# Kernel optimization log

Hardware: AMD Instinct MI355X
Metric: run time of the kernel (lower is better)

## Reference

```python
import jax, jax.numpy as jnp
import numpy as np

N, IN, WS, OUT, H = 50000, 256, 128, 32, 4
E, M, K = 800000, 2, 10
D = OUT * H  # 128
NEG_SLOPE = 0.2


def _decay(n, alpha=1.5):
    k = np.arange(1, n + 1)
    x = 1.0 / np.power(k, alpha)
    return (x / x.sum()).astype(np.float32)


def setup_inputs() -> dict:
    key = jax.random.key(0)
    ks = jax.random.split(key, 16)
    h = jax.random.normal(ks[0], (N, IN), dtype=jnp.float32)
    src0 = jax.random.randint(ks[1], (E,), 0, N, dtype=jnp.int32)
    dst0 = jax.random.randint(ks[2], (E,), 0, N, dtype=jnp.int32)
    src1 = jax.random.randint(ks[3], (E,), 0, N, dtype=jnp.int32)
    dst1 = jax.random.randint(ks[4], (E,), 0, N, dtype=jnp.int32)
    s = 0.05
    Wh = jax.random.normal(ks[5], (WS, IN), dtype=jnp.float32) * s
    # layer 0 (per metapath): fc (H*F, WS), attn_l/attn_r (H, F)
    fc0 = jax.random.normal(ks[6], (M, H * OUT, WS), dtype=jnp.float32) * s
    al0 = jax.random.normal(ks[7], (M, H, OUT), dtype=jnp.float32) * s
    ar0 = jax.random.normal(ks[8], (M, H, OUT), dtype=jnp.float32) * s
    # layer 1 (per metapath): fc (H*F, H*F)
    fc1 = jax.random.normal(ks[9], (M, H * OUT, H * OUT), dtype=jnp.float32) * s
    al1 = jax.random.normal(ks[10], (M, H, OUT), dtype=jnp.float32) * s
    ar1 = jax.random.normal(ks[11], (M, H, OUT), dtype=jnp.float32) * s
    Wp1 = jax.random.normal(ks[12], (128, D), dtype=jnp.float32) * s
    bp1 = jnp.zeros((128,), dtype=jnp.float32)
    Wp2 = jax.random.normal(ks[13], (1, 128), dtype=jnp.float32) * s
    return dict(h=h, src0=src0, dst0=dst0, src1=src1, dst1=dst1, Wh=Wh,
                fc0=fc0, al0=al0, ar0=ar0, fc1=fc1, al1=al1, ar1=ar1,
                Wp1=Wp1, bp1=bp1, Wp2=Wp2)


def gat_layer(x, src, dst, fcW, attn_l, attn_r):
    # x: (N, Din); fcW: (H*F, Din)
    ft = (x @ fcW.T).reshape(N, H, OUT)            # (N, H, F)
    el = jnp.sum(ft * attn_l, axis=-1)             # (N, H)
    er = jnp.sum(ft * attn_r, axis=-1)             # (N, H)
    e = jax.nn.leaky_relu(el[src] + er[dst], NEG_SLOPE)  # (E, H)
    # edge softmax over incoming edges of each destination node
    mx = jax.ops.segment_max(e, dst, num_segments=N)     # (N, H)
    ee = jnp.exp(e - mx[dst])
    sm = jax.ops.segment_sum(ee, dst, num_segments=N)    # (N, H)
    a = ee / sm[dst]                                     # (E, H)
    # global top-k over the edge dimension (th.topk dim=0), per head
    scores, idx = jax.lax.top_k(a.T, K)                  # (H, K)
    scores = jax.nn.softmax(scores, axis=-1)             # softmax over k
    a_new = jnp.zeros_like(a).at[idx, jnp.arange(H)[:, None]].set(scores)
    msg = ft[src] * a_new[:, :, None]                    # (E, H, F)
    out = jax.ops.segment_sum(msg, dst, num_segments=N)  # (N, H, F)
    return jax.nn.elu(out).reshape(N, H * OUT)


def reference(h, src0, dst0, src1, dst1, Wh, fc0, al0, ar0, fc1, al1, ar1, Wp1, bp1, Wp2):
    c = _decay(2, 1.5)
    wh = h @ Wh.T  # (N, WS)
    srcs = (src0, src1)
    dsts = (dst0, dst1)
    embs = []
    for i in range(M):
        a = gat_layer(wh, srcs[i], dsts[i], fc0[i], al0[i], ar0[i])  # (N, D)
        b = gat_layer(a, srcs[i], dsts[i], fc1[i], al1[i], ar1[i])   # (N, D)
        embs.append(a * c[0] + b * c[1])
    z = jnp.stack(embs, axis=1)                                      # (N, M, D)
    w = jnp.tanh(z @ Wp1.T + bp1) @ Wp2.T                            # (N, M, 1)
    beta = jax.nn.softmax(w, axis=1)
    return jnp.sum(beta * z, axis=1)                                 # (N, D)
```

## Files before the change

### kernel.cpp

```cpp
#include <hip/hip_runtime.h>
#include <math.h>

#define NN   50000
#define IN_F 256
#define OUTF 32
#define NH   4
#define NE   800000
#define NM   2
#define NK   10
#define ND   128

#define NCB  782
#define CCAP 1280
#define DSH  6
#define DMSK 63
#define NSL  32
#define SLW  245

__device__ __forceinline__ float lrelu(float x){ return x >= 0.f ? x : 0.2f*x; }
__device__ __forceinline__ unsigned fmap(float f){
  unsigned u = __float_as_uint(f);
  return (u & 0x80000000u) ? ~u : (u | 0x80000000u);
}
__device__ __forceinline__ float funmap(unsigned u){
  return (u & 0x80000000u) ? __uint_as_float(u & 0x7FFFFFFFu) : __uint_as_float(~u);
}

__global__ __launch_bounds__(256) void k_plpr(
    const float* __restrict__ fc0, const float* __restrict__ al0, const float* __restrict__ ar0,
    const float* __restrict__ fc1, const float* __restrict__ al1, const float* __restrict__ ar1,
    float* __restrict__ plpr)
{
  int idx = blockIdx.x*256 + threadIdx.x;
  if (idx >= 4096) return;
  int w  = idx & 127;
  int hh = (idx >> 7) & 3;
  int lr = (idx >> 9) & 1;
  int m  = (idx >> 10) & 1;
  int L  = (idx >> 11) & 1;
  const float* fc = L ? fc1 : fc0;
  const float* at = L ? (lr ? ar1 : al1) : (lr ? ar0 : al0);
  float s = 0.f;
  for (int f = 0; f < OUTF; f++)
    s += at[(m*NH + hh)*OUTF + f] * fc[((size_t)m*128 + hh*OUTF + f)*128 + w];
  plpr[idx] = s;
}

__global__ __launch_bounds__(256) void k_p2(
    const float* __restrict__ plpr, const float* __restrict__ Whm, float* __restrict__ P2)
{
  int idx = blockIdx.x*256 + threadIdx.x;
  if (idx >= 16*256) return;
  int q = idx >> 8, k = idx & 255;
  float s = 0.f;
  for (int w = 0; w < 128; w++)
    s += plpr[q*128 + w] * Whm[(size_t)w*IN_F + k];
  P2[q*256 + k] = s;
}

__global__ __launch_bounds__(256) void k_el(
    const float* __restrict__ hmat, const float* __restrict__ P2,
    float* __restrict__ el0, float* __restrict__ er0)
{
  __shared__ float hs[64][68];
  __shared__ float PL2[16][260];
  int tid = threadIdx.x;
  int r0 = blockIdx.x * 64;
  for (int i = tid; i < 16*64; i += 256){
    int q = i >> 6, k4 = i & 63;
    float4 v = ((const float4*)P2)[q*64 + k4];
    *(float4*)&PL2[q][k4*4] = v;
  }
  int r = tid >> 2, c = tid & 3;
  float a0 = 0.f, a1 = 0.f, a2 = 0.f, a3 = 0.f;
  for (int kc = 0; kc < IN_F; kc += 64){
#pragma unroll
    for (int it = 0; it < 4; it++){
      int item = it*256 + tid;
      int row = item >> 4, f4 = item & 15;
      int grow = r0 + row;
      float4 v = make_float4(0.f,0.f,0.f,0.f);
      if (grow < NN) v = ((const float4*)hmat)[(size_t)grow*64 + (kc >> 2) + f4];
      *(float4*)&hs[row][f4*4] = v;
    }
    __syncthreads();
#pragma unroll
    for (int k4 = 0; k4 < 16; k4++){
      float4 hv = *(const float4*)&hs[r][k4*4];
      float4 u0 = *(const float4*)&PL2[c*4+0][kc + k4*4];
      float4 u1 = *(const float4*)&PL2[c*4+1][kc + k4*4];
      float4 u2 = *(const float4*)&PL2[c*4+2][kc + k4*4];
      float4 u3 = *(const float4*)&PL2[c*4+3][kc + k4*4];
      a0 += hv.x*u0.x; a0 += hv.y*u0.y; a0 += hv.z*u0.z; a0 += hv.w*u0.w;
      a1 += hv.x*u1.x; a1 += hv.y*u1.y; a1 += hv.z*u1.z; a1 += hv.w*u1.w;
      a2 += hv.x*u2.x; a2 += hv.y*u2.y; a2 += hv.z*u2.z; a2 += hv.w*u2.w;
      a3 += hv.x*u3.x; a3 += hv.y*u3.y; a3 += hv.z*u3.z; a3 += hv.w*u3.w;
    }
    __syncthreads();
  }
  int row = r0 + r;
  if (row < NN){
    int m = c >> 1;
    float* dp = (c & 1) ? er0 : el0;
    *(float4*)&dp[((size_t)m*NN + row)*4] = make_float4(a0, a1, a2, a3);
  }
}

__global__ __launch_bounds__(256) void k_part(
    const int* __restrict__ s0, const int* __restrict__ d0,
    const int* __restrict__ s1, const int* __restrict__ d1,
    unsigned* __restrict__ ccnt, unsigned long long* __restrict__ coarse)
{
  int m = blockIdx.y;
  const int* sp = m ? s1 : s0;
  const int* dp = m ? d1 : d0;
  __shared__ unsigned hist[NCB], base[NCB], cur[NCB];
  int tid = threadIdx.x;
  for (int j = tid; j < NCB; j += 256){ hist[j] = 0u; cur[j] = 0u; }
  __syncthreads();
  int per = (NE + gridDim.x - 1) / gridDim.x;
  int e0 = blockIdx.x * per;
  int e1 = e0 + per; if (e1 > NE) e1 = NE;
  for (int i = e0 + tid; i < e1; i += 256)
    atomicAdd(&hist[dp[i] >> DSH], 1u);
  __syncthreads();
  for (int j = tid; j < NCB; j += 256)
    base[j] = hist[j] ? atomicAdd(&ccnt[m*NCB + j], hist[j]) : 0u;
  __syncthreads();
  for (int i = e0 + tid; i < e1; i += 256){
    int d = dp[i];
    int b = d >> DSH;
    unsigned loc = atomicAdd(&cur[b], 1u);
    unsigned pos = base[b] + loc;
    if (pos < CCAP)
      coarse[((size_t)m*NCB + b)*CCAP + pos] =
          ((unsigned long long)(unsigned)i << 24)
        | ((unsigned long long)(unsigned)(d & DMSK) << 16)
        | (unsigned long long)(unsigned)sp[i];
  }
}

__global__ __launch_bounds__(256) void k_fused(
    const unsigned* __restrict__ ccnt, const unsigned long long* __restrict__ coarse,
    const float* __restrict__ el, const float* __restrict__ er,
    unsigned long long* __restrict__ cand)
{
  int bb = blockIdx.x, m = blockIdx.y;
  const unsigned long long* ce = coarse + ((size_t)m*NCB + bb)*CCAP;
  unsigned cnt = ccnt[m*NCB + bb]; if (cnt > CCAP) cnt = CCAP;
  const float* elp = el + (size_t)m*NN*4;
  const float* erp = er + (size_t)m*NN*4;
  int tid = threadIdx.x;
  int h = tid & 3, es = tid >> 2;
  int dbase = bb << DSH;

  __shared__ float4 erL[64];
  __shared__ unsigned mxL[64][4];
  __shared__ unsigned long long smL[64][4];
  __shared__ unsigned metaL[CCAP];
  __shared__ unsigned long long smem_u64[CCAP*2];
  float* eL = (float*)smem_u64;
  unsigned long long (*cs)[NK] = (unsigned long long(*)[NK])smem_u64;

  if (tid < 64){
    int d = dbase + tid;
    erL[tid] = (d < NN) ? *(const float4*)&erp[(size_t)d*4] : make_float4(0.f,0.f,0.f,0.f);
  }
  { int j = tid; mxL[j>>2][j&3] = 0u; smL[j>>2][j&3] = 0ULL; }
  __syncthreads();

  {
    unsigned p = es;
    for (; p + 192 < cnt; p += 256){
      unsigned long long v0 = ce[p], v1 = ce[p+64], v2 = ce[p+128], v3 = ce[p+192];
      float g0 = elp[(unsigned)(v0 & 0xFFFFULL)*4 + h];
      float g1 = elp[(unsigned)(v1 & 0xFFFFULL)*4 + h];
      float g2 = elp[(unsigned)(v2 & 0xFFFFULL)*4 + h];
      float g3 = elp[(unsigned)(v3 & 0xFFFFULL)*4 + h];
      unsigned d0 = (unsigned)((v0 >> 16) & 0xFFULL);
      unsigned d1 = (unsigned)((v1 >> 16) & 0xFFULL);
      unsigned d2 = (unsigned)((v2 >> 16) & 0xFFULL);
      unsigned d3 = (unsigned)((v3 >> 16) & 0xFFULL);
      float e0 = lrelu(g0 + ((const float*)&erL[d0])[h]);
      float e1 = lrelu(g1 + ((const float*)&erL[d1])[h]);
      float e2 = lrelu(g2 + ((const float*)&erL[d2])[h]);
      float e3 = lrelu(g3 + ((const float*)&erL[d3])[h]);
      eL[p*4 + h] = e0; eL[(p+64)*4 + h] = e1;
      eL[(p+128)*4 + h] = e2; eL[(p+192)*4 + h] = e3;
      if (h == 0){
        metaL[p]     = ((unsigned)(v0 >> 24) << 8) | d0;
        metaL[p+64]  = ((unsigned)(v1 >> 24) << 8) | d1;
        metaL[p+128] = ((unsigned)(v2 >> 24) << 8) | d2;
        metaL[p+192] = ((unsigned)(v3 >> 24) << 8) | d3;
      }
      atomicMax(&mxL[d0][h], fmap(e0));
      atomicMax(&mxL[d1][h], fmap(e1));
      atomicMax(&mxL[d2][h], fmap(e2));
      atomicMax(&mxL[d3][h], fmap(e3));
    }
    for (; p < cnt; p += 64){
      unsigned long long v = ce[p];
      unsigned src  = (unsigned)(v & 0xFFFFULL);
      unsigned dloc = (unsigned)((v >> 16) & 0xFFULL);
      float e = lrelu(elp[src*4 + h] + ((const float*)&erL[dloc])[h]);
      eL[p*4 + h] = e;
      if (h == 0) metaL[p] = ((unsigned)(v >> 24) << 8) | dloc;
      atomicMax(&mxL[dloc][h], fmap(e));
    }
  }
  __syncthreads();

  for (unsigned p = es; p < cnt; p += 64){
    unsigned dloc = metaL[p] & 255u;
    float e = eL[p*4 + h];
    float texp = expf(e - funmap(mxL[dloc][h]));
    eL[p*4 + h] = texp;
    atomicAdd(&smL[dloc][h],
        (unsigned long long)llrint((double)texp * 1073741824.0));
  }
  __syncthreads();

  unsigned long long top[NK];
#pragma unroll
  for (int k = 0; k < NK; k++) top[k] = 0ULL;
  for (unsigned p = es; p < cnt; p += 64){
    unsigned mt = metaL[p];
    unsigned dloc = mt & 255u;
    unsigned eid  = mt >> 8;
    float texp = eL[p*4 + h];
    float smv = (float)((double)smL[dloc][h] * (1.0/1073741824.0));
    float av = texp / smv;
    unsigned long long key = ((unsigned long long)__float_as_uint(av) << 32)
                           | (unsigned long long)(~eid);
    if (key > top[NK-1]){
#pragma unroll
      for (int k = 0; k < NK; k++){
        unsigned long long hi = key > top[k] ? key : top[k];
        unsigned long long lo = key > top[k] ? top[k] : key;
        top[k] = hi; key = lo;
      }
    }
  }
  __syncthreads();

  int row = h*64 + es;
#pragma unroll
  for (int k = 0; k < NK; k++) cs[row][k] = top[k];
  __syncthreads();
  int w = tid >> 6, lane = tid & 63;
  unsigned long long mytop[NK];
#pragma unroll
  for (int k = 0; k < NK; k++) mytop[k] = cs[w*64 + lane][k];
  unsigned long long best = 0ULL; int bp = -1;
#pragma unroll
  for (int k = 0; k < NK; k++) if (mytop[k] > best){ best = mytop[k]; bp = k; }
  for (int r = 0; r < NK; r++){
    unsigned long long b = best; int srcl = lane;
#pragma unroll
    for (int off = 32; off > 0; off >>= 1){
      unsigned long long ob = __shfl_down(b, off, 64);
      int os = __shfl_down(srcl, off, 64);
      if (ob > b){ b = ob; srcl = os; }
    }
    b = __shfl(b, 0, 64); srcl = __shfl(srcl, 0, 64);
    if (lane == 0) cand[(((size_t)m*NH + w)*NCB + blockIdx.x)*NK + r] = b;
    if (lane == srcl && bp >= 0){
#pragma unroll
      for (int k = 0; k < NK; k++) if (k == bp) mytop[k] = 0ULL;
      best = 0ULL; bp = -1;
#pragma unroll
      for (int k = 0; k < NK; k++) if (mytop[k] > best){ best = mytop[k]; bp = k; }
    }
  }
}

__global__ __launch_bounds__(256) void k_merge1(
    const unsigned long long* __restrict__ cand,
    unsigned long long* __restrict__ cand2)
{
  int hh = blockIdx.x, m = blockIdx.y, z = blockIdx.z;
  int tid = threadIdx.x;
  const unsigned long long* cp = cand + ((size_t)m*NH + hh)*((size_t)NCB*NK);
  int start = z*SLW;
  int end = start + SLW; if (end > NCB*NK) end = NCB*NK;
  unsigned long long mykey = (start + tid < end) ? cp[start + tid] : 0ULL;

  __shared__ unsigned long long red[256];
  __shared__ int redpos[256];
  for (int r = 0; r < NK; r++){
    red[tid] = mykey; redpos[tid] = tid;
    __syncthreads();
    for (int st = 128; st > 0; st >>= 1){
      if (tid < st && red[tid+st] > red[tid]){ red[tid] = red[tid+st]; redpos[tid] = redpos[tid+st]; }
      __syncthreads();
    }
    if (tid == 0)
      cand2[(((size_t)m*NH + hh)*NSL + z)*NK + r] = red[0];
    int winner = redpos[0];
    __syncthreads();
    if (tid == winner) mykey = 0ULL;
  }
}

__global__ __launch_bounds__(512) void k_merge2(
    const unsigned long long* __restrict__ cand2,
    unsigned long long* __restrict__ selg)
{
  int hh = blockIdx.x, m = blockIdx.y;
  int tid = threadIdx.x;
  const unsigned long long* cp = cand2 + ((size_t)m*NH + hh)*((size_t)NSL*NK);
  unsigned long long mykey = (tid < NSL*NK) ? cp[tid] : 0ULL;

  __shared__ unsigned long long red[512];
  __shared__ int redpos[512];
  for (int r = 0; r < NK; r++){
    red[tid] = mykey; redpos[tid] = tid;
    __syncthreads();
    for (int st = 256; st > 0; st >>= 1){
      if (tid < st && red[tid+st] > red[tid]){ red[tid] = red[tid+st]; redpos[tid] = redpos[tid+st]; }
      __syncthreads();
    }
    if (tid == 0)
      selg[((size_t)m*NH + hh)*NK + r] = red[0];
    int winner = redpos[0];
    __syncthreads();
    if (tid == winner) mykey = 0ULL;
  }
}

__global__ __launch_bounds__(256) void k_selA(
    const unsigned long long* __restrict__ selg,
    const int* __restrict__ s0, const int* __restrict__ d0,
    const int* __restrict__ s1, const int* __restrict__ d1,
    const int* __restrict__ idsA,
    int* __restrict__ idsOut, int4* __restrict__ selinfo, int layer)
{
  int m = blockIdx.x;
  int tid = threadIdx.x;
  const int* sp = m ? s1 : s0;
  const int* dp = m ? d1 : d0;
  int wv = tid >> 6, lane = tid & 63;

  __shared__ float scL[NH][NK];
  __shared__ int snL[NH][NK], dL[NH][NK];
  __shared__ int slotOf[NH][NK], srcOf[NH][NK];

  if (tid < NH*NK){
    int h = tid / NK, k = tid % NK;
    unsigned long long s = selg[((size_t)m*NH + h)*NK + k];
    int e = (int)(~(unsigned)(s & 0xFFFFFFFFULL));
    snL[h][k] = sp[e];
    dL[h][k]  = dp[e];
  }
  __syncthreads();

  if (tid < NH){
    float v0 = __uint_as_float((unsigned)(selg[((size_t)m*NH + tid)*NK + 0] >> 32));
    float p[NK]; float sum = 0.f;
#pragma unroll
    for (int k = 0; k < NK; k++){
      float v = __uint_as_float((unsigned)(selg[((size_t)m*NH + tid)*NK + k] >> 32));
      p[k] = expf(v - v0); sum += p[k];
    }
#pragma unroll
    for (int k = 0; k < NK; k++) scL[tid][k] = p[k] / sum;
  }

  if (wv == 0){
    int myA = -1;
    if (layer) myA = idsA[m*64 + lane];
    int myid = -1;
    int cnt = 0;
    for (int h = 0; h < NH; h++){
      for (int k = 0; k < NK; k++){
        int sn = snL[h][k], d = dL[h][k];
        int srcslot = sn;
        bool ok = true;
        if (layer){
          unsigned long long mb = __ballot(myA == sn);
          if (mb) srcslot = __ffsll(mb) - 1;
          else ok = false;
        }
        int slot = -1;
        if (ok){
          unsigned long long mm = __ballot(lane < cnt && myid == d);
          if (mm) slot = __ffsll(mm) - 1;
          else { slot = cnt; if (lane == cnt) myid = d; cnt++; }
        }
        if (lane == 0){ slotOf[h][k] = slot; srcOf[h][k] = srcslot; }
      }
    }
    idsOut[m*64 + lane] = (lane < cnt) ? myid : -1;
  }
  __syncthreads();

  if (tid < NH*NK){
    int h = tid / NK, k = tid % NK;
    selinfo[((size_t)m*NH + h)*NK + k] =
        make_int4(snL[h][k], slotOf[h][k], srcOf[h][k], __float_as_int(scL[h][k]));
  }
}

__global__ __launch_bounds__(256) void k_selB(
    const int4* __restrict__ selinfo,
    const float* __restrict__ hmat, const float* __restrict__ Whm,
    const float* __restrict__ ftsrc,
    const float* __restrict__ fcW,
    float* __restrict__ valsOut, int layer)
{
  int h = blockIdx.x, m = blockIdx.y;
  int tid = threadIdx.x;
  __shared__ int sn10[NK], slot10[NK], srcsl10[NK];
  __shared__ float sc10[NK];
  __shared__ float hs10[NK][260];
  __shared__ float whL10[NK][132];
  __shared__ float dsumL[NK][32];

  if (tid < NK){
    int4 si = selinfo[((size_t)m*NH + h)*NK + tid];
    sn10[tid] = si.x; slot10[tid] = si.y; srcsl10[tid] = si.z;
    sc10[tid] = __int_as_float(si.w);
  }
  __syncthreads();

  if (layer == 0){
    for (int t = tid; t < NK*64; t += 256){
      int e = t >> 6, k4 = t & 63;
      float4 v = ((const float4*)hmat)[(size_t)sn10[e]*64 + k4];
      *(float4*)&hs10[e][k4*4] = v;
    }
    __syncthreads();
    int w = tid & 127, rh = tid >> 7;
    float acc5[5];
#pragma unroll
    for (int i = 0; i < 5; i++) acc5[i] = 0.f;
    const float4* wp = (const float4*)&Whm[(size_t)w*IN_F];
    for (int k4 = 0; k4 < 64; k4++){
      float4 wv2 = wp[k4];
#pragma unroll
      for (int i = 0; i < 5; i++){
        float4 hv = *(const float4*)&hs10[rh + 2*i][k4*4];
        acc5[i] += hv.x*wv2.x; acc5[i] += hv.y*wv2.y;
        acc5[i] += hv.z*wv2.z; acc5[i] += hv.w*wv2.w;
      }
    }
#pragma unroll
    for (int i = 0; i < 5; i++) whL10[rh + 2*i][w] = acc5[i];
    __syncthreads();
  }

  for (int t = tid; t < NK*32; t += 256){
    int k = t >> 5, f = t & 31;
    float dsum = 0.f;
    if (slot10[k] >= 0){
      const float* x = layer ? (ftsrc + ((size_t)m*64 + srcsl10[k])*128) : &whL10[k][0];
      const float* wr = fcW + ((size_t)m*128 + h*OUTF + f)*128;
      for (int w = 0; w < 128; w++) dsum += x[w] * wr[w];
    }
    dsumL[k][f] = dsum;
  }
  __syncthreads();

  if (tid < OUTF){
    int f = tid;
    float* vals = valsOut + (size_t)m*64*128;
    for (int k = 0; k < NK; k++){
      int slot = slot10[k];
      if (slot < 0) continue;
      vals[(size_t)slot*128 + h*OUTF + f] += sc10[k] * dsumL[k][f];
    }
  }
}

__global__ __launch_bounds__(128) void k_elu2(
    const int* __restrict__ ids, float* __restrict__ vals,
    const float* __restrict__ plpr1,
    float* __restrict__ el2, float* __restrict__ er2, int doEl2)
{
  int slot = blockIdx.x, m = blockIdx.y, tid = threadIdx.x;
  float* row = vals + ((size_t)m*64 + slot)*128;
  float x = row[tid];
  row[tid] = x > 0.f ? x : expm1f(x);
  __syncthreads();
  if (!doEl2) return;
  int d = ids[m*64 + slot];
  if (d < 0) return;
  if (tid < 8){
    int lr = tid >> 2, hh = tid & 3;
    const float* P = plpr1 + (((size_t)m*2 + lr)*NH + hh)*128;
    float s = 0.f;
    for (int w = 0; w < 128; w++) s += row[w] * P[w];
    float* dp = lr ? er2 : el2;
    dp[((size_t)m*NN + d)*4 + hh] = s;
  }
}

__global__ __launch_bounds__(128) void k_final(
    const int* __restrict__ ids, const float* __restrict__ vals,
    const float* __restrict__ Wp1, const float* __restrict__ bp1, const float* __restrict__ Wp2,
    float c0, float c1, float* __restrict__ out)
{
  int j = blockIdx.x;
  int n = ids[j];
  if (n < 0) return;
  for (int q = 0; q < j; q++) if (ids[q] == n) return;
  int tid = threadIdx.x;
  __shared__ float z[2][128];
  __shared__ int slots[4];
  if (tid < 4){
    int sl = -1;
    const int* base = ids + tid*64;
    for (int q = 0; q < 64; q++) if (base[q] == n){ sl = q; break; }
    slots[tid] = sl;
  }
  __syncthreads();
#pragma unroll
  for (int m = 0; m < 2; m++){
    int sa = slots[m], sb = slots[2 + m];
    float av = sa >= 0 ? vals[((size_t)m*64 + sa)*128 + tid] : 0.f;
    float bv = sb >= 0 ? vals[((size_t)(2 + m)*64 + sb)*128 + tid] : 0.f;
    z[m][tid] = c0*av + c1*bv;
  }
  __syncthreads();
  float a0 = bp1[tid], a1 = a0;
  const float* wr = Wp1 + (size_t)tid*128;
  for (int w = 0; w < 128; w++){
    float wv = wr[w];
    a0 += z[0][w]*wv;
    a1 += z[1][w]*wv;
  }
  float t0 = tanhf(a0), t1 = tanhf(a1);
  float w2v = Wp2[tid];
  __shared__ float r0[128], r1[128];
  r0[tid] = t0*w2v; r1[tid] = t1*w2v;
  __syncthreads();
  for (int st = 64; st > 0; st >>= 1){
    if (tid < st){ r0[tid] += r0[tid+st]; r1[tid] += r1[tid+st]; }
    __syncthreads();
  }
  __shared__ float b0s, b1s;
  if (tid == 0){
    float w0 = r0[0], w1 = r1[0];
    float mxv = fmaxf(w0, w1);
    float e0 = expf(w0 - mxv), e1 = expf(w1 - mxv);
    float s = e0 + e1;
    b0s = e0/s; b1s = e1/s;
  }
  __syncthreads();
  out[(size_t)n*ND + tid] = b0s*z[0][tid] + b1s*z[1][tid];
}

extern "C" void kernel_launch(void* const* d_in, const int* in_sizes, int n_in,
                              void* d_out, int out_size, void* d_ws, size_t ws_size,
                              hipStream_t stream)
{
  const float* h    = (const float*)d_in[0];
  const int*   src0 = (const int*)d_in[1];
  const int*   dst0 = (const int*)d_in[2];
  const int*   src1 = (const int*)d_in[3];
  const int*   dst1 = (const int*)d_in[4];
  const float* Wh   = (const float*)d_in[5];
  const float* fc0  = (const float*)d_in[6];
  const float* al0  = (const float*)d_in[7];
  const float* ar0  = (const float*)d_in[8];
  const float* fc1  = (const float*)d_in[9];
  const float* al1  = (const float*)d_in[10];
  const float* ar1  = (const float*)d_in[11];
  const float* Wp1  = (const float*)d_in[12];
  const float* bp1  = (const float*)d_in[13];
  const float* Wp2  = (const float*)d_in[14];
  float* out = (float*)d_out;

  char* ws = (char*)d_ws;
  size_t off = 0;
  auto alloc = [&](size_t b){ size_t o = off; off = (off + b + 255) & ~(size_t)255; return o; };
  size_t o_el0    = alloc((size_t)NM*NN*4*4);
  size_t o_er0    = alloc((size_t)NM*NN*4*4);
  size_t o_plpr   = alloc(4096*4);
  size_t o_p2     = alloc(16*256*4);
  size_t o_cand   = alloc((size_t)NM*NH*NCB*NK*8);
  size_t o_cand2  = alloc((size_t)NM*NH*NSL*NK*8);
  size_t o_selg   = alloc((size_t)NM*NH*NK*8);
  size_t o_selinf = alloc((size_t)NM*NH*NK*16);
  size_t o_coarse = alloc((size_t)NM*NCB*CCAP*8);
  size_t o_zs     = off;
  size_t o_ccnt   = alloc((size_t)NM*NCB*4);
  size_t o_el2    = alloc((size_t)NM*NN*4*4);
  size_t o_er2    = alloc((size_t)NM*NN*4*4);
  size_t o_vals   = alloc((size_t)2*NM*64*128*4);
  size_t zlen = off - o_zs;
  size_t o_ids    = alloc((size_t)2*NM*64*4);
  (void)ws_size; (void)in_sizes; (void)n_in;

  float* el0p  = (float*)(ws + o_el0);
  float* er0p  = (float*)(ws + o_er0);
  float* plprp = (float*)(ws + o_plpr);
  float* p2p   = (float*)(ws + o_p2);
  unsigned long long* candp  = (unsigned long long*)(ws + o_cand);
  unsigned long long* cand2p = (unsigned long long*)(ws + o_cand2);
  unsigned long long* selgp  = (unsigned long long*)(ws + o_selg);
  int4* selinfp = (int4*)(ws + o_selinf);
  unsigned long long* coarsep = (unsigned long long*)(ws + o_coarse);
  unsigned* ccntp = (unsigned*)(ws + o_ccnt);
  float* el2p  = (float*)(ws + o_el2);
  float* er2p  = (float*)(ws + o_er2);
  float* valsp = (float*)(ws + o_vals);
  int*   idsp  = (int*)(ws + o_ids);
  float* vals0p = valsp;
  float* vals1p = valsp + (size_t)NM*64*128;
  int* ids0p = idsp;
  int* ids1p = idsp + NM*64;
  float* plpr1p = plprp + 2048;

  double x1 = 1.0 / (2.0 * sqrt(2.0));
  double ssum = 1.0 + x1;
  float c0 = (float)(1.0/ssum), c1 = (float)(x1/ssum);

  hipMemsetAsync(d_out, 0, (size_t)out_size*sizeof(float), stream);
  hipMemsetAsync(ws + o_zs, 0, zlen, stream);

  k_plpr<<<16, 256, 0, stream>>>(fc0, al0, ar0, fc1, al1, ar1, plprp);
  k_p2<<<16, 256, 0, stream>>>(plprp, Wh, p2p);
  k_el<<<(NN + 63)/64, 256, 0, stream>>>(h, p2p, el0p, er0p);

  k_part<<<dim3(128, NM), 256, 0, stream>>>(src0, dst0, src1, dst1, ccntp, coarsep);

  dim3 gf(NCB, NM);
  dim3 gm1(NH, NM, NSL);
  dim3 gm2(NH, NM);
  dim3 gb(NH, NM);
  dim3 ge(64, NM);

  k_fused<<<gf, 256, 0, stream>>>(ccntp, coarsep, el0p, er0p, candp);
  k_merge1<<<gm1, 256, 0, stream>>>(candp, cand2p);
  k_merge2<<<gm2, 512, 0, stream>>>(cand2p, selgp);
  k_selA<<<NM, 256, 0, stream>>>(selgp, src0, dst0, src1, dst1,
                                 (const int*)nullptr, ids0p, selinfp, 0);
  k_selB<<<gb, 256, 0, stream>>>(selinfp, h, Wh, (const float*)nullptr, fc0, vals0p, 0);
  k_elu2<<<ge, 128, 0, stream>>>(ids0p, vals0p, plpr1p, el2p, er2p, 1);

  k_fused<<<gf, 256, 0, stream>>>(ccntp, coarsep, el2p, er2p, candp);
  k_merge1<<<gm1, 256, 0, stream>>>(candp, cand2p);
  k_merge2<<<gm2, 512, 0, stream>>>(cand2p, selgp);
  k_selA<<<NM, 256, 0, stream>>>(selgp, src0, dst0, src1, dst1,
                                 ids0p, ids1p, selinfp, 1);
  k_selB<<<gb, 256, 0, stream>>>(selinfp, h, Wh, vals0p, fc1, vals1p, 1);
  k_elu2<<<ge, 128, 0, stream>>>(ids1p, vals1p, plpr1p, el2p, er2p, 0);

  k_final<<<256, 128, 0, stream>>>(idsp, valsp, Wp1, bp1, Wp2, c0, c1, out);
}
```

Baseline: 299.4 us.

## Exploit layer-1 sparsity: use constant background attention for non-selected sources

Adds a layer-1 variant of the fused edge-softmax/top-k kernel. It exploits the fact that after layer 0 only up to 64 nodes per metapath have nonzero features, so el for every other source is zero. Edges from non-selected sources share one background score per destination, which is computed once, and only edges from selected sources (marked in a shared bitmap) get individually gathered scores. This removes most per-edge gathers and exp calls, in exchange for extra shared memory and a capped sparse list (256 entries) that could overflow silently.

```diff
diff --git a/kernel.cpp b/kernel.cpp
--- a/kernel.cpp
+++ b/kernel.cpp
@@ -16,6 +16,7 @@
 #define DMSK 63
 #define NSL  32
 #define SLW  245
+#define SPCAP 256
 
 __device__ __forceinline__ float lrelu(float x){ return x >= 0.f ? x : 0.2f*x; }
 __device__ __forceinline__ unsigned fmap(float f){
@@ -274,6 +275,151 @@
   }
 }
 
+__global__ __launch_bounds__(256) void k_fused2(
+    const unsigned* __restrict__ ccnt, const unsigned long long* __restrict__ coarse,
+    const float* __restrict__ el2g, const float* __restrict__ er2g,
+    const int* __restrict__ idsA,
+    unsigned long long* __restrict__ cand)
+{
+  int bb = blockIdx.x, m = blockIdx.y;
+  const unsigned long long* ce = coarse + ((size_t)m*NCB + bb)*CCAP;
+  int cnt = (int)ccnt[m*NCB + bb]; if (cnt > CCAP) cnt = CCAP;
+  const float* elp = el2g + (size_t)m*NN*4;
+  const float* erp = er2g + (size_t)m*NN*4;
+  int tid = threadIdx.x;
+  int dbase = bb << DSH;
+
+  __shared__ unsigned sbm[1568];
+  __shared__ float4 erL[64];
+  __shared__ unsigned cntL[64], spCntD[64];
+  __shared__ unsigned char spIdx[CCAP];
+  __shared__ int spSrc[SPCAP], spDl[SPCAP], spCnt;
+  __shared__ float mxF[64][4], smvF[64][4], avBg[64][4];
+  __shared__ float avSp[SPCAP][4];
+  __shared__ unsigned long long cs[256][NK];
+
+  for (int i = tid; i < 1568; i += 256) sbm[i] = 0u;
+  if (tid < 64){
+    cntL[tid] = 0u; spCntD[tid] = 0u;
+    int d = dbase + tid;
+    erL[tid] = (d < NN) ? *(const float4*)&erp[(size_t)d*4] : make_float4(0.f,0.f,0.f,0.f);
+  }
+  if (tid == 0) spCnt = 0;
+  __syncthreads();
+  if (tid < 64){
+    int v = idsA[m*64 + tid];
+    if (v >= 0) atomicOr(&sbm[v >> 5], 1u << (v & 31));
+  }
+  __syncthreads();
+
+  for (int p = tid; p < cnt; p += 256){
+    unsigned long long v = ce[p];
+    unsigned src  = (unsigned)(v & 0xFFFFULL);
+    unsigned dloc = (unsigned)((v >> 16) & 0xFFULL);
+    atomicAdd(&cntL[dloc], 1u);
+    unsigned char si = 255;
+    if ((sbm[src >> 5] >> (src & 31)) & 1u){
+      int j = atomicAdd(&spCnt, 1);
+      if (j < SPCAP){
+        spSrc[j] = (int)src; spDl[j] = (int)dloc;
+        si = (unsigned char)j;
+        atomicAdd(&spCntD[dloc], 1u);
+      }
+    }
+    spIdx[p] = si;
+  }
+  __syncthreads();
+
+  int nsp = spCnt < SPCAP ? spCnt : SPCAP;
+  {
+    int dloc = tid >> 2, h = tid & 3;
+    float erv = ((const float*)&erL[dloc])[h];
+    float ebg = lrelu(0.f + erv);
+    int nbg = (int)cntL[dloc] - (int)spCntD[dloc];
+    float mx = (nbg > 0) ? ebg : -INFINITY;
+    for (int j = 0; j < nsp; j++)
+      if (spDl[j] == dloc)
+        mx = fmaxf(mx, lrelu(elp[(size_t)spSrc[j]*4 + h] + erv));
+    unsigned long long sm = 0ULL;
+    float tbg = 0.f;
+    if (nbg > 0){
+      tbg = expf(ebg - mx);
+      sm += (unsigned long long)nbg *
+            (unsigned long long)llrint((double)tbg * 1073741824.0);
+    }
+    for (int j = 0; j < nsp; j++)
+      if (spDl[j] == dloc){
+        float es_ = lrelu(elp[(size_t)spSrc[j]*4 + h] + erv);
+        sm += (unsigned long long)llrint((double)expf(es_ - mx) * 1073741824.0);
+      }
+    float smv = (float)((double)sm * (1.0/1073741824.0));
+    mxF[dloc][h] = mx; smvF[dloc][h] = smv;
+    avBg[dloc][h] = (cntL[dloc] > 0 && nbg > 0) ? (tbg / smv) : 0.f;
+  }
+  __syncthreads();
+  for (int t = tid; t < nsp*4; t += 256){
+    int j = t >> 2, h = t & 3;
+    int dloc = spDl[j];
+    float erv = ((const float*)&erL[dloc])[h];
+    float es_ = lrelu(elp[(size_t)spSrc[j]*4 + h] + erv);
+    avSp[j][h] = expf(es_ - mxF[dloc][h]) / smvF[dloc][h];
+  }
+  __syncthreads();
+
+  int h = tid & 3, es = tid >> 2;
+  unsigned long long top[NK];
+#pragma unroll
+  for (int k = 0; k < NK; k++) top[k] = 0ULL;
+  for (int p = es; p < cnt; p += 64){
+    unsigned long long v = ce[p];
+    unsigned dloc = (unsigned)((v >> 16) & 0xFFULL);
+    unsigned eid  = (unsigned)(v >> 24);
+    unsigned char si = spIdx[p];
+    float av = (si == 255) ? avBg[dloc][h] : avSp[si][h];
+    unsigned long long key = ((unsigned long long)__float_as_uint(av) << 32)
+                           | (unsigned long long)(~eid);
+    if (key > top[NK-1]){
+#pragma unroll
+      for (int k = 0; k < NK; k++){
+        unsigned long long hi = key > top[k] ? key : top[k];
+        unsigned long long lo = key > top[k] ? top[k] : key;
+        top[k] = hi; key = lo;
+      }
+    }
+  }
+  __syncthreads();
+
+  int row = h*64 + es;
+#pragma unroll
+  for (int k = 0; k < NK; k++) cs[row][k] = top[k];
+  __syncthreads();
+  int w = tid >> 6, lane = tid & 63;
+  unsigned long long mytop[NK];
+#pragma unroll
+  for (int k = 0; k < NK; k++) mytop[k] = cs[w*64 + lane][k];
+  unsigned long long best = 0ULL; int bp = -1;
+#pragma unroll
+  for (int k = 0; k < NK; k++) if (mytop[k] > best){ best = mytop[k]; bp = k; }
+  for (int r = 0; r < NK; r++){
+    unsigned long long b = best; int srcl = lane;
+#pragma unroll
+    for (int off = 32; off > 0; off >>= 1){
+      unsigned long long ob = __shfl_down(b, off, 64);
+      int os = __shfl_down(srcl, off, 64);
+      if (ob > b){ b = ob; srcl = os; }
+    }
+    b = __shfl(b, 0, 64); srcl = __shfl(srcl, 0, 64);
+    if (lane == 0) cand[(((size_t)m*NH + w)*NCB + blockIdx.x)*NK + r] = b;
+    if (lane == srcl && bp >= 0){
+#pragma unroll
+      for (int k = 0; k < NK; k++) if (k == bp) mytop[k] = 0ULL;
+      best = 0ULL; bp = -1;
+#pragma unroll
+      for (int k = 0; k < NK; k++) if (mytop[k] > best){ best = mytop[k]; bp = k; }
+    }
+  }
+}
+
 __global__ __launch_bounds__(256) void k_merge1(
     const unsigned long long* __restrict__ cand,
     unsigned long long* __restrict__ cand2)
@@ -639,7 +785,7 @@
   k_selB<<<gb, 256, 0, stream>>>(selinfp, h, Wh, (const float*)nullptr, fc0, vals0p, 0);
   k_elu2<<<ge, 128, 0, stream>>>(ids0p, vals0p, plpr1p, el2p, er2p, 1);
 
-  k_fused<<<gf, 256, 0, stream>>>(ccntp, coarsep, el2p, er2p, candp);
+  k_fused2<<<gf, 256, 0, stream>>>(ccntp, coarsep, el2p, er2p, ids0p, candp);
   k_merge1<<<gm1, 256, 0, stream>>>(candp, cand2p);
   k_merge2<<<gm2, 512, 0, stream>>>(cand2p, selgp);
   k_selA<<<NM, 256, 0, stream>>>(selgp, src0, dst0, src1, dst1,
```

Result: faster. 285.0 us (-4.8%).
